# Optimization experiments

Measured on AMD Instinct MI355X. Metric: run time of the kernel, lower is better.

## Reference

```python
import jax, jax.numpy as jnp
import numpy as np

B, N, D, H = 4, 256, 256, 8
HD = D // H
DFF = 4 * D
EPS = 1e-5


def setup_inputs() -> dict:
    key = jax.random.key(0)
    ks = jax.random.split(key, 12)
    s = 0.02
    p = lambda k, shape: (jax.random.normal(k, shape, jnp.float32) * s)
    return dict(
        h=jax.random.normal(ks[0], (B, N, D), jnp.float32),
        e=jax.random.normal(ks[1], (B, N, N, D), jnp.float32),
        We=p(ks[2], (D, D)), be=jnp.zeros((D,), jnp.float32),
        Ws=p(ks[3], (D, D)), bs=jnp.zeros((D,), jnp.float32),
        Wd=p(ks[4], (D, D)), bd=jnp.zeros((D,), jnp.float32),
        Wb=p(ks[5], (D, H)), bb=jnp.zeros((H,), jnp.float32),
        ln1_g=jnp.ones((D,), jnp.float32), ln1_b=jnp.zeros((D,), jnp.float32),
        Wqkv=p(ks[6], (D, 3 * D)), bqkv=jnp.zeros((3 * D,), jnp.float32),
        Wo=p(ks[7], (D, D)), bo=jnp.zeros((D,), jnp.float32),
        ln2_g=jnp.ones((D,), jnp.float32), ln2_b=jnp.zeros((D,), jnp.float32),
        W1=p(ks[8], (D, DFF)), b1=jnp.zeros((DFF,), jnp.float32),
        W2=p(ks[9], (DFF, D)), b2=jnp.zeros((D,), jnp.float32),
    )


def _ln(x, g, b):
    m = jnp.mean(x, axis=-1, keepdims=True)
    v = jnp.mean((x - m) ** 2, axis=-1, keepdims=True)
    return (x - m) * jax.lax.rsqrt(v + EPS) * g + b


def reference(h, e, We, be, Ws, bs, Wd, bd, Wb, bb, ln1_g, ln1_b,
              Wqkv, bqkv, Wo, bo, ln2_g, ln2_b, W1, b1, W2, b2):
    # Edge update: broadcast-add of src/dst node projections + ReLU over [B,N,N,D]
    e_new = jax.nn.relu(e @ We + be
                        + (h @ Ws + bs)[:, :, None, :]   # src -> unsqueeze(2)
                        + (h @ Wd + bd)[:, None, :, :])  # dst -> unsqueeze(1)
    # Per-head additive attention bias [B,H,N,N]
    bias = jnp.einsum('bijd,dh->bhij', e_new, Wb) + bb[None, :, None, None]
    # Pre-LN self-attention with additive bias (torch MHA, eval mode)
    x = _ln(h, ln1_g, ln1_b)
    qkv = x @ Wqkv + bqkv
    q, k, v = jnp.split(qkv, 3, axis=-1)
    q = q.reshape(B, N, H, HD)
    k = k.reshape(B, N, H, HD)
    v = v.reshape(B, N, H, HD)
    scores = jnp.einsum('bihd,bjhd->bhij', q, k) / np.float32(np.sqrt(HD)) + bias
    attn = jax.nn.softmax(scores, axis=-1)
    o = jnp.einsum('bhij,bjhd->bihd', attn, v).reshape(B, N, D)
    h1 = h + (o @ Wo + bo)
    # Pre-LN FFN (exact GELU, as torch nn.GELU default)
    y = _ln(h1, ln2_g, ln2_b)
    h2 = h1 + (jax.nn.gelu(y @ W1 + b1, approximate=False) @ W2 + b2)
    return (h2, e_new)
```

## Files before the change

kernel.cpp:

```cpp
#include <hip/hip_runtime.h>
#include <math.h>

#define EPS 1e-5f

typedef __attribute__((ext_vector_type(4))) float floatx4;
typedef __attribute__((ext_vector_type(8))) short shortx8;

__device__ __forceinline__ unsigned short f2bf(float f){
  union { float f; unsigned u; } v; v.f = f;
  unsigned r = v.u + 0x7FFFu + ((v.u >> 16) & 1u);
  return (unsigned short)(r >> 16);
}
__device__ __forceinline__ float bf2f(unsigned short s){
  union { unsigned u; float f; } v; v.u = ((unsigned)s) << 16;
  return v.f;
}

__global__ __launch_bounds__(256) void k_prep(
    const float* __restrict__ We, const float* __restrict__ Ws, const float* __restrict__ Wd,
    const float* __restrict__ Wqkv, const float* __restrict__ Wo, const float* __restrict__ W1,
    const float* __restrict__ W2, const float* __restrict__ Wb,
    unsigned short* __restrict__ WeT, unsigned short* __restrict__ WsT,
    unsigned short* __restrict__ WdT, unsigned short* __restrict__ WqkvT,
    unsigned short* __restrict__ WoT, unsigned short* __restrict__ W1T,
    unsigned short* __restrict__ W2T, unsigned short* __restrict__ WbT16)
{
  const int blk = blockIdx.x, tid = threadIdx.x;
  if (blk == 240){
#pragma unroll
    for (int hh=0; hh<8; hh++) WbT16[hh*256+tid] = f2bf(Wb[tid*8+hh]);
#pragma unroll
    for (int hh=8; hh<16; hh++) WbT16[hh*256+tid] = 0;
    return;
  }
  const float* src; unsigned short* dst; int K, N, t;
  if (blk < 16)      { src=We;   dst=WeT;   K=256;  N=256;  t=blk; }
  else if (blk < 32) { src=Ws;   dst=WsT;   K=256;  N=256;  t=blk-16; }
  else if (blk < 48) { src=Wd;   dst=WdT;   K=256;  N=256;  t=blk-32; }
  else if (blk < 96) { src=Wqkv; dst=WqkvT; K=256;  N=768;  t=blk-48; }
  else if (blk < 112){ src=Wo;   dst=WoT;   K=256;  N=256;  t=blk-96; }
  else if (blk < 176){ src=W1;   dst=W1T;   K=256;  N=1024; t=blk-112; }
  else               { src=W2;   dst=W2T;   K=1024; N=256;  t=blk-176; }
  const int tpr = N >> 6;
  const int k0 = (t / tpr) << 6, n0 = (t % tpr) << 6;
  __shared__ float tile[64][65];
#pragma unroll
  for (int s=0;s<16;s++){ int f=tid+(s<<8); int r=f>>6, c=f&63;
    tile[r][c] = src[(size_t)(k0+r)*N + n0 + c]; }
  __syncthreads();
#pragma unroll
  for (int s=0;s<16;s++){ int f=tid+(s<<8); int r=f>>6, c=f&63;
    dst[(size_t)(n0+r)*K + k0 + c] = f2bf(tile[c][r]); }
}

__global__ __launch_bounds__(256) void k_front(
  const float* __restrict__ h, const float* __restrict__ g1, const float* __restrict__ b1l,
  const float* __restrict__ bs, const float* __restrict__ be, const float* __restrict__ bd,
  const float* __restrict__ bqkv,
  const unsigned short* __restrict__ WsT, const unsigned short* __restrict__ WdT,
  const unsigned short* __restrict__ WqkvT,
  float* __restrict__ S, float* __restrict__ T,
  unsigned short* __restrict__ Qb, unsigned short* __restrict__ Kb,
  unsigned short* __restrict__ VTb)
{
  __shared__ float hs[16][256];
  __shared__ __align__(16) unsigned short xa[16*264];
  __shared__ float red1[16][16], red2[16][16];
  __shared__ float rmean[16], rinv[16];
  const int tid = threadIdx.x;
  const int rb = blockIdx.x & 63;
  const int chunk = blockIdx.x >> 6;
  const int row0 = rb * 16;
  const int b = row0 >> 8;
  const int w = tid>>6, l = tid&63, lrow = l&15, quad = l>>4;

#pragma unroll
  for (int s=0;s<4;s++){
    int f = tid + s*256; int r = f>>6, c4 = f&63;
    float4 v = ((const float4*)(h + (size_t)row0*256))[f];
    *(float4*)(&hs[r][c4*4]) = v;
  }
  __syncthreads();
  {
    int row = tid>>4, l16 = tid&15;
    if (chunk >= 2){
      float sm=0.f, sq=0.f;
#pragma unroll
      for (int j=0;j<16;j++){ float v=hs[row][l16*16+j]; sm+=v; sq+=v*v; }
      red1[row][l16]=sm; red2[row][l16]=sq;
      __syncthreads();
      if (l16==0){
        float s0=0.f,q0=0.f;
#pragma unroll
        for(int k=0;k<16;k++){ s0+=red1[row][k]; q0+=red2[row][k]; }
        float m=s0*(1.f/256.f);
        rmean[row]=m; rinv[row]=rsqrtf(q0*(1.f/256.f)-m*m+EPS);
      }
      __syncthreads();
      float m=rmean[row], iv=rinv[row];
#pragma unroll
      for (int j=0;j<16;j++){ int col=l16*16+j;
        xa[row*264+col] = f2bf((hs[row][col]-m)*iv*g1[col] + b1l[col]); }
    } else {
#pragma unroll
      for (int j=0;j<16;j++){ int col=l16*16+j; xa[row*264+col] = f2bf(hs[row][col]); }
    }
  }
  __syncthreads();
  const unsigned short* Wt;
  if (chunk==0) Wt = WsT; else if (chunk==1) Wt = WdT;
  else Wt = WqkvT + (size_t)(chunk-2)*256*256;
  floatx4 a4[4];
#pragma unroll
  for (int t=0;t<4;t++) a4[t] = (floatx4){0.f,0.f,0.f,0.f};
  for (int c=0;c<8;c++){
    shortx8 af = *(const shortx8*)(xa + lrow*264 + c*32 + quad*8);
#pragma unroll
    for (int t=0;t<4;t++){
      int n = (w*4+t)*16 + lrow;
      shortx8 bf = *(const shortx8*)(Wt + (size_t)n*256 + c*32 + quad*8);
      a4[t] = __builtin_amdgcn_mfma_f32_16x16x32_bf16(af, bf, a4[t], 0, 0, 0);
    }
  }
#pragma unroll
  for (int t=0;t<4;t++){
    int ct = w*4+t;
#pragma unroll
    for (int reg=0;reg<4;reg++){
      int row = quad*4+reg, col = ct*16+lrow;
      float v = a4[t][reg];
      if (chunk==0) S[(size_t)(row0+row)*256+col] = v + bs[col] + be[col];
      else if (chunk==1) T[(size_t)(row0+row)*256+col] = v + bd[col];
      else if (chunk==2){ float q = v + bqkv[col]; int hh=col>>5, d=col&31;
        Qb[((size_t)(b*8+hh)*256 + (row0&255)+row)*32 + d] = f2bf(q); }
      else if (chunk==3){ float q = v + bqkv[256+col]; int hh=col>>5, d=col&31;
        Kb[((size_t)(b*8+hh)*256 + (row0&255)+row)*32 + d] = f2bf(q); }
      else { float q = v + bqkv[512+col]; int hh=col>>5, d=col&31;
        VTb[((size_t)(b*8+hh)*32 + d)*256 + (row0&255)+row] = f2bf(q); }
    }
  }
}

__global__ __launch_bounds__(256) void k_edge(
    const float* __restrict__ e, const unsigned short* __restrict__ WeT,
    const float* __restrict__ S, const float* __restrict__ T,
    const unsigned short* __restrict__ WbTg,
    float* __restrict__ eo, float* __restrict__ bias)
{
  __shared__ __align__(16) unsigned short smem[16896];
  __shared__ float sbuf[256];
  __shared__ __align__(16) unsigned short WbT[4096];
  unsigned short* As = smem;
  unsigned short* Bs = smem + 2560;
  unsigned short* En = smem;

  const int tid = threadIdx.x;
  const int blk = blockIdx.x;
  const int jt = blk & 3;
  const int i  = (blk >> 2) & 255;
  const int b  = blk >> 10;
  const int j0 = jt * 64;
  const int w = tid >> 6, l = tid & 63;
  const int lrow = l & 15, quad = l >> 4;

  sbuf[tid] = S[((b << 8) + i) * 256 + tid];
  ((uint4*)WbT)[tid]       = ((const uint4*)WbTg)[tid];
  ((uint4*)WbT)[tid + 256] = ((const uint4*)WbTg)[tid + 256];

  floatx4 acc[16];
#pragma unroll
  for (int t = 0; t < 16; t++) acc[t] = (floatx4){0.f,0.f,0.f,0.f};

  const float* eBase = e + ((size_t)((b*256 + i)*256 + j0)) * 256;
  const int rA = tid >> 3, qA = tid & 7;
  const int nB0 = tid >> 2, segB = tid & 2 ? 0 : 0; (void)segB;

  float4 pa0 = *(const float4*)(eBase + rA*256 + qA*4);
  float4 pa1 = *(const float4*)(eBase + (rA+32)*256 + qA*4);
  uint4 pb[4];
#pragma unroll
  for (int s=0;s<4;s++){ int f = tid + s*256; int n = f>>2, seg = f&3;
    pb[s] = *(const uint4*)(WeT + n*256 + seg*8); }
  {
    unsigned short* d0 = As + rA*40 + qA*4;
    d0[0]=f2bf(pa0.x); d0[1]=f2bf(pa0.y); d0[2]=f2bf(pa0.z); d0[3]=f2bf(pa0.w);
    unsigned short* d1 = As + (rA+32)*40 + qA*4;
    d1[0]=f2bf(pa1.x); d1[1]=f2bf(pa1.y); d1[2]=f2bf(pa1.z); d1[3]=f2bf(pa1.w);
#pragma unroll
    for (int s=0;s<4;s++){ int f = tid + s*256; int n = f>>2, seg = f&3;
      *(uint4*)(Bs + n*40 + seg*8) = pb[s]; }
  }
  __syncthreads();

  for (int c = 0; c < 8; c++){
    if (c < 7){
      const int k0n = (c+1)*32;
      pa0 = *(const float4*)(eBase + rA*256 + k0n + qA*4);
      pa1 = *(const float4*)(eBase + (rA+32)*256 + k0n + qA*4);
#pragma unroll
      for (int s=0;s<4;s++){ int f = tid + s*256; int n = f>>2, seg = f&3;
        pb[s] = *(const uint4*)(WeT + n*256 + k0n + seg*8); }
    }
    shortx8 af = *(const shortx8*)(As + (w*16 + lrow)*40 + quad*8);
#pragma unroll
    for (int t = 0; t < 16; t++){
      shortx8 bfr = *(const shortx8*)(Bs + (t*16 + lrow)*40 + quad*8);
      acc[t] = __builtin_amdgcn_mfma_f32_16x16x32_bf16(af, bfr, acc[t], 0, 0, 0);
    }
    __syncthreads();
    if (c < 7){
      unsigned short* d0 = As + rA*40 + qA*4;
      d0[0]=f2bf(pa0.x); d0[1]=f2bf(pa0.y); d0[2]=f2bf(pa0.z); d0[3]=f2bf(pa0.w);
      unsigned short* d1 = As + (rA+32)*40 + qA*4;
      d1[0]=f2bf(pa1.x); d1[1]=f2bf(pa1.y); d1[2]=f2bf(pa1.z); d1[3]=f2bf(pa1.w);
#pragma unroll
      for (int s=0;s<4;s++){ int f = tid + s*256; int n = f>>2, seg = f&3;
        *(uint4*)(Bs + n*40 + seg*8) = pb[s]; }
    }
    __syncthreads();
  }
  const float* Tb = T + (size_t)(b*256 + j0) * 256;
#pragma unroll
  for (int reg = 0; reg < 4; reg++){
    int rloc = w*16 + quad*4 + reg;
    const float* Trow = Tb + rloc*256;
#pragma unroll
    for (int t = 0; t < 16; t++){
      int col = t*16 + lrow;
      float v = acc[t][reg] + sbuf[col] + Trow[col];
      v = fmaxf(v, 0.f);
      En[rloc*264 + col] = f2bf(v);
    }
  }
  __syncthreads();
  float* eop = eo + ((size_t)((b*256 + i)*256 + j0)) * 256;
#pragma unroll
  for (int s = 0; s < 16; s++){
    int fi = tid + s*256;
    int r = fi >> 6, c4 = fi & 63;
    const unsigned short* src = En + r*264 + c4*4;
    float4 v = { bf2f(src[0]), bf2f(src[1]), bf2f(src[2]), bf2f(src[3]) };
    *(float4*)(eop + r*256 + c4*4) = v;
  }
  floatx4 accb = (floatx4){0.f,0.f,0.f,0.f};
#pragma unroll
  for (int c = 0; c < 8; c++){
    int k0 = c*32;
    shortx8 af = *(const shortx8*)(En + (w*16 + lrow)*264 + k0 + quad*8);
    shortx8 bfrag = *(const shortx8*)(WbT + lrow*256 + k0 + quad*8);
    accb = __builtin_amdgcn_mfma_f32_16x16x32_bf16(af, bfrag, accb, 0, 0, 0);
  }
  if (lrow < 8){
    float* bp = bias + ((size_t)((b*8 + lrow)*256 + i)) * 256;
    int jb = j0 + w*16 + quad*4;
#pragma unroll
    for (int r = 0; r < 4; r++) bp[jb + r] = accb[r];
  }
}


__global__ __launch_bounds__(256) void k_attn(
  const unsigned short* __restrict__ Qb, const unsigned short* __restrict__ Kb,
  const unsigned short* __restrict__ VTb, const float* __restrict__ bias,
  const float* __restrict__ bbv, unsigned short* __restrict__ Ob)
{
  __shared__ __align__(16) unsigned short Qa[32*40];
  __shared__ __align__(16) unsigned short Kl[256*40];
  __shared__ __align__(16) unsigned short Vt[32*264];
  __shared__ __align__(16) unsigned short Pl[32*264];
  __shared__ float srowm[4][16], srows[4][16], sinv[32];

  const int tid = threadIdx.x;
  const int ic = blockIdx.x & 7, bh = blockIdx.x >> 3;
  const int i0 = ic * 32;
  const int w = tid>>6, l = tid&63, lrow = l&15, quad = l>>4;

  if (tid < 128){
    int r = tid>>2, cseg = tid&3;
    *(uint4*)(Qa + r*40 + cseg*8) = ((const uint4*)(Qb + (size_t)(bh*256+i0)*32))[tid];
  }
#pragma unroll
  for (int s=0;s<4;s++){
    int f = tid + s*256; int r = f>>2, cseg = f&3;
    *(uint4*)(Kl + r*40 + cseg*8) = ((const uint4*)(Kb + (size_t)bh*8192))[f];
  }
#pragma unroll
  for (int s=0;s<4;s++){
    int f = tid + s*256; int r = f>>5, c8 = f&31;
    *(uint4*)(Vt + r*264 + c8*8) = ((const uint4*)(VTb + (size_t)bh*8192))[f];
  }
  __syncthreads();

  const int rt = w & 1, cs = (w>>1)*8;
  const float bbh = bbv[bh & 7];
  floatx4 sc[8];
  {
    shortx8 aq = *(const shortx8*)(Qa + (rt*16+lrow)*40 + quad*8);
    floatx4 z = (floatx4){0.f,0.f,0.f,0.f};
#pragma unroll
    for (int t=0;t<8;t++){
      shortx8 bk = *(const shortx8*)(Kl + ((cs+t)*16+lrow)*40 + quad*8);
      sc[t] = __builtin_amdgcn_mfma_f32_16x16x32_bf16(aq, bk, z, 0, 0, 0);
    }
  }
  const float scale = 0.17677669529663687f;
  float mx[4] = {-1e30f,-1e30f,-1e30f,-1e30f};
#pragma unroll
  for (int t=0;t<8;t++){
#pragma unroll
    for (int reg=0;reg<4;reg++){
      size_t bidx = ((size_t)(bh*256 + i0 + rt*16 + quad*4 + reg))*256 + (cs+t)*16 + lrow;
      float v = sc[t][reg]*scale + bias[bidx] + bbh;
      sc[t][reg] = v;
      mx[reg] = fmaxf(mx[reg], v);
    }
  }
#pragma unroll
  for (int m=1;m<16;m<<=1){
#pragma unroll
    for (int reg=0;reg<4;reg++) mx[reg] = fmaxf(mx[reg], __shfl_xor(mx[reg], m));
  }
  if (lrow == 0){
#pragma unroll
    for (int reg=0;reg<4;reg++) srowm[w][quad*4+reg] = mx[reg];
  }
  __syncthreads();
  float sum[4] = {0.f,0.f,0.f,0.f};
#pragma unroll
  for (int reg=0;reg<4;reg++){
    float gm = fmaxf(srowm[w][quad*4+reg], srowm[w^2][quad*4+reg]);
#pragma unroll
    for (int t=0;t<8;t++){
      float p = __expf(sc[t][reg] - gm);
      sc[t][reg] = p; sum[reg] += p;
    }
  }
#pragma unroll
  for (int m=1;m<16;m<<=1){
#pragma unroll
    for (int reg=0;reg<4;reg++) sum[reg] += __shfl_xor(sum[reg], m);
  }
  if (lrow == 0){
#pragma unroll
    for (int reg=0;reg<4;reg++) srows[w][quad*4+reg] = sum[reg];
  }
#pragma unroll
  for (int t=0;t<8;t++){
#pragma unroll
    for (int reg=0;reg<4;reg++)
      Pl[(rt*16+quad*4+reg)*264 + (cs+t)*16 + lrow] = f2bf(sc[t][reg]);
  }
  __syncthreads();
  if (lrow == 0 && w < 2){
#pragma unroll
    for (int reg=0;reg<4;reg++){
      int row = rt*16 + quad*4 + reg;
      sinv[row] = 1.f/(srows[w][quad*4+reg] + srows[w^2][quad*4+reg]);
    }
  }
  __syncthreads();
  const int rt2 = w & 1, ctd = w >> 1;
  floatx4 oc = (floatx4){0.f,0.f,0.f,0.f};
#pragma unroll
  for (int kc=0;kc<8;kc++){
    shortx8 ap = *(const shortx8*)(Pl + (rt2*16+lrow)*264 + kc*32 + quad*8);
    shortx8 bv = *(const shortx8*)(Vt + (ctd*16+lrow)*264 + kc*32 + quad*8);
    oc = __builtin_amdgcn_mfma_f32_16x16x32_bf16(ap, bv, oc, 0, 0, 0);
  }
  const int bq = bh >> 3, hh = bh & 7;
#pragma unroll
  for (int reg=0;reg<4;reg++){
    int row = rt2*16 + quad*4 + reg;
    int d = ctd*16 + lrow;
    Ob[((size_t)(bq*256 + i0 + row))*256 + hh*32 + d] = f2bf(oc[reg]*sinv[row]);
  }
}

__global__ __launch_bounds__(256) void k_back(
  const unsigned short* __restrict__ Ob, const unsigned short* __restrict__ WoT,
  const float* __restrict__ bo, const float* __restrict__ h,
  const float* __restrict__ g2, const float* __restrict__ b2l,
  const unsigned short* __restrict__ W1T, const float* __restrict__ b1f,
  const unsigned short* __restrict__ W2T, const float* __restrict__ b2f,
  float* __restrict__ out)
{
  __shared__ __align__(16) unsigned short Os[16*264];
  __shared__ float h1s[16*264];
  __shared__ __align__(16) unsigned short ys[16*264];
  __shared__ __align__(16) unsigned short Gs[16*1032];
  __shared__ float red1[16][16], red2[16][16];
  __shared__ float rmean[16], rinv[16];

  const int tid = threadIdx.x;
  const int row0 = blockIdx.x * 16;
  const int w = tid>>6, l = tid&63, lrow = l&15, quad = l>>4;

#pragma unroll
  for (int s=0;s<2;s++){
    int f = tid + s*256; int r = f>>5, c8 = f&31;
    *(uint4*)(Os + r*264 + c8*8) = ((const uint4*)(Ob + (size_t)row0*256))[f];
  }
  __syncthreads();
  {
    floatx4 a4[4];
#pragma unroll
    for (int t=0;t<4;t++) a4[t] = (floatx4){0.f,0.f,0.f,0.f};
    for (int c=0;c<8;c++){
      shortx8 af = *(const shortx8*)(Os + lrow*264 + c*32 + quad*8);
#pragma unroll
      for (int t=0;t<4;t++){
        int n = (w*4+t)*16 + lrow;
        shortx8 bf = *(const shortx8*)(WoT + (size_t)n*256 + c*32 + quad*8);
        a4[t] = __builtin_amdgcn_mfma_f32_16x16x32_bf16(af, bf, a4[t], 0, 0, 0);
      }
    }
#pragma unroll
    for (int t=0;t<4;t++){
#pragma unroll
      for (int reg=0;reg<4;reg++){
        int row = quad*4+reg, col = (w*4+t)*16+lrow;
        h1s[row*264+col] = a4[t][reg] + bo[col] + h[(size_t)(row0+row)*256 + col];
      }
    }
  }
  __syncthreads();
  {
    int row = tid>>4, l16 = tid&15;
    float sm=0.f, sq=0.f;
#pragma unroll
    for (int j=0;j<16;j++){ float v = h1s[row*264 + l16*16 + j]; sm+=v; sq+=v*v; }
    red1[row][l16]=sm; red2[row][l16]=sq;
    __syncthreads();
    if (l16==0){
      float s0=0.f,q0=0.f;
#pragma unroll
      for (int k=0;k<16;k++){ s0+=red1[row][k]; q0+=red2[row][k]; }
      float m = s0*(1.f/256.f);
      rmean[row]=m; rinv[row]=rsqrtf(q0*(1.f/256.f)-m*m+EPS);
    }
    __syncthreads();
    float m = rmean[row], iv = rinv[row];
#pragma unroll
    for (int j=0;j<16;j++){ int col = l16*16+j;
      ys[row*264+col] = f2bf((h1s[row*264+col]-m)*iv*g2[col] + b2l[col]); }
  }
  __syncthreads();
  {
    floatx4 a4[16];
#pragma unroll
    for (int t=0;t<16;t++) a4[t] = (floatx4){0.f,0.f,0.f,0.f};
    for (int c=0;c<8;c++){
      shortx8 af = *(const shortx8*)(ys + lrow*264 + c*32 + quad*8);
#pragma unroll
      for (int t=0;t<16;t++){
        int n = (w*16+t)*16 + lrow;
        shortx8 bf = *(const shortx8*)(W1T + (size_t)n*256 + c*32 + quad*8);
        a4[t] = __builtin_amdgcn_mfma_f32_16x16x32_bf16(af, bf, a4[t], 0, 0, 0);
      }
    }
#pragma unroll
    for (int t=0;t<16;t++){
#pragma unroll
      for (int reg=0;reg<4;reg++){
        int row = quad*4+reg, col = (w*16+t)*16+lrow;
        float v = a4[t][reg] + b1f[col];
        float ge = 0.5f*v*(1.f + erff(v*0.70710678118654752f));
        Gs[row*1032+col] = f2bf(ge);
      }
    }
  }
  __syncthreads();
  {
    floatx4 a4[4];
#pragma unroll
    for (int t=0;t<4;t++) a4[t] = (floatx4){0.f,0.f,0.f,0.f};
    for (int c=0;c<32;c++){
      shortx8 af = *(const shortx8*)(Gs + lrow*1032 + c*32 + quad*8);
#pragma unroll
      for (int t=0;t<4;t++){
        int n = (w*4+t)*16 + lrow;
        shortx8 bf = *(const shortx8*)(W2T + (size_t)n*1024 + c*32 + quad*8);
        a4[t] = __builtin_amdgcn_mfma_f32_16x16x32_bf16(af, bf, a4[t], 0, 0, 0);
      }
    }
#pragma unroll
    for (int t=0;t<4;t++){
#pragma unroll
      for (int reg=0;reg<4;reg++){
        int row = quad*4+reg, col = (w*4+t)*16+lrow;
        out[(size_t)(row0+row)*256+col] = h1s[row*264+col] + a4[t][reg] + b2f[col];
      }
    }
  }
}

extern "C" void kernel_launch(void* const* d_in, const int* in_sizes, int n_in,
                              void* d_out, int out_size, void* d_ws, size_t ws_size,
                              hipStream_t stream)
{
  (void)in_sizes; (void)n_in; (void)out_size; (void)ws_size;
  const float* h    = (const float*)d_in[0];
  const float* e    = (const float*)d_in[1];
  const float* We   = (const float*)d_in[2];
  const float* be   = (const float*)d_in[3];
  const float* Ws   = (const float*)d_in[4];
  const float* bs   = (const float*)d_in[5];
  const float* Wd   = (const float*)d_in[6];
  const float* bd   = (const float*)d_in[7];
  const float* Wb   = (const float*)d_in[8];
  const float* bb   = (const float*)d_in[9];
  const float* g1   = (const float*)d_in[10];
  const float* b1l  = (const float*)d_in[11];
  const float* Wqkv = (const float*)d_in[12];
  const float* bqkv = (const float*)d_in[13];
  const float* Wo   = (const float*)d_in[14];
  const float* bo   = (const float*)d_in[15];
  const float* g2   = (const float*)d_in[16];
  const float* b2l  = (const float*)d_in[17];
  const float* W1   = (const float*)d_in[18];
  const float* b1f  = (const float*)d_in[19];
  const float* W2   = (const float*)d_in[20];
  const float* b2f  = (const float*)d_in[21];

  float* out  = (float*)d_out;
  float* h2_o = out;
  float* e_o  = out + 262144;

  float* wsf = (float*)d_ws;
  unsigned short* ush = (unsigned short*)d_ws;
  unsigned short* WeT   = ush;
  unsigned short* WsT   = ush + 65536;
  unsigned short* WdT   = ush + 131072;
  unsigned short* WqkvT = ush + 196608;
  unsigned short* WoT   = ush + 393216;
  unsigned short* W1T   = ush + 458752;
  unsigned short* W2T   = ush + 720896;
  unsigned short* WbT16 = ush + 983040;
  float* S_   = wsf + 493568;
  float* T_   = wsf + 755712;
  float* bias = wsf + 1017856;
  unsigned short* Qb  = (unsigned short*)(wsf + 3115008);
  unsigned short* Kb  = (unsigned short*)(wsf + 3246080);
  unsigned short* VTb = (unsigned short*)(wsf + 3377152);
  unsigned short* Ob  = (unsigned short*)(wsf + 3508224);

  k_prep <<<dim3(241),  dim3(256), 0, stream>>>(We,Ws,Wd,Wqkv,Wo,W1,W2,Wb,
                                                WeT,WsT,WdT,WqkvT,WoT,W1T,W2T,WbT16);
  k_front<<<dim3(320),  dim3(256), 0, stream>>>(h, g1,b1l, bs,be,bd, bqkv,
                                                WsT,WdT,WqkvT, S_,T_, Qb,Kb,VTb);
  k_edge <<<dim3(4096), dim3(256), 0, stream>>>(e, WeT, S_, T_, WbT16, e_o, bias);
  k_attn <<<dim3(256),  dim3(256), 0, stream>>>(Qb, Kb, VTb, bias, bb, Ob);
  k_back <<<dim3(64),   dim3(256), 0, stream>>>(Ob, WoT, bo, h, g2,b2l,
                                                W1T,b1f, W2T,b2f, h2_o);
}
```

Before: 668.6 us.

## Stream edge tiles straight into MFMA registers without LDS staging in k_edge

Rewrites the edge GEMM so each lane loads its own fp32 slice of e, converts it to bf16 in registers and uses it directly as the MFMA operand. The bf16 weight fragments are read straight from global memory instead of being staged in shared memory. With the operand roles swapped, each lane owns contiguous output columns, so the ReLU'd edge output is written as fp32 float4 with no bf16 round-trip through LDS, and the block-wide barriers disappear. LDS shrinks to the per-wave bias tile and launch bounds request 3 blocks per CU; the cost is strided per-lane global loads and repeated weight reads that rely on cache hits.

```diff
diff --git a/kernel.cpp b/kernel.cpp
--- a/kernel.cpp
+++ b/kernel.cpp
@@ -141,18 +141,13 @@
   }
 }
 
-__global__ __launch_bounds__(256) void k_edge(
+__global__ __launch_bounds__(256, 3) void k_edge(
     const float* __restrict__ e, const unsigned short* __restrict__ WeT,
     const float* __restrict__ S, const float* __restrict__ T,
     const unsigned short* __restrict__ WbTg,
     float* __restrict__ eo, float* __restrict__ bias)
 {
-  __shared__ __align__(16) unsigned short smem[16896];
-  __shared__ float sbuf[256];
-  __shared__ __align__(16) unsigned short WbT[4096];
-  unsigned short* As = smem;
-  unsigned short* Bs = smem + 2560;
-  unsigned short* En = smem;
+  __shared__ __align__(16) unsigned short En[64*264];
 
   const int tid = threadIdx.x;
   const int blk = blockIdx.x;
@@ -162,92 +157,60 @@
   const int j0 = jt * 64;
   const int w = tid >> 6, l = tid & 63;
   const int lrow = l & 15, quad = l >> 4;
-
-  sbuf[tid] = S[((b << 8) + i) * 256 + tid];
-  ((uint4*)WbT)[tid]       = ((const uint4*)WbTg)[tid];
-  ((uint4*)WbT)[tid + 256] = ((const uint4*)WbTg)[tid + 256];
+  const int jloc = w*16 + lrow;
+
+  const float* eRow = e + ((size_t)((b*256 + i)*256 + j0 + jloc)) * 256 + quad*8;
+  const float* Trow = T + ((size_t)(b*256 + j0 + jloc)) * 256;
+  const float* Srow = S + ((size_t)(b*256 + i)) * 256;
+  const unsigned short* wBase = WeT + lrow*256 + quad*8;
 
   floatx4 acc[16];
 #pragma unroll
   for (int t = 0; t < 16; t++) acc[t] = (floatx4){0.f,0.f,0.f,0.f};
 
-  const float* eBase = e + ((size_t)((b*256 + i)*256 + j0)) * 256;
-  const int rA = tid >> 3, qA = tid & 7;
-  const int nB0 = tid >> 2, segB = tid & 2 ? 0 : 0; (void)segB;
-
-  float4 pa0 = *(const float4*)(eBase + rA*256 + qA*4);
-  float4 pa1 = *(const float4*)(eBase + (rA+32)*256 + qA*4);
-  uint4 pb[4];
-#pragma unroll
-  for (int s=0;s<4;s++){ int f = tid + s*256; int n = f>>2, seg = f&3;
-    pb[s] = *(const uint4*)(WeT + n*256 + seg*8); }
-  {
-    unsigned short* d0 = As + rA*40 + qA*4;
-    d0[0]=f2bf(pa0.x); d0[1]=f2bf(pa0.y); d0[2]=f2bf(pa0.z); d0[3]=f2bf(pa0.w);
-    unsigned short* d1 = As + (rA+32)*40 + qA*4;
-    d1[0]=f2bf(pa1.x); d1[1]=f2bf(pa1.y); d1[2]=f2bf(pa1.z); d1[3]=f2bf(pa1.w);
-#pragma unroll
-    for (int s=0;s<4;s++){ int f = tid + s*256; int n = f>>2, seg = f&3;
-      *(uint4*)(Bs + n*40 + seg*8) = pb[s]; }
-  }
-  __syncthreads();
-
-  for (int c = 0; c < 8; c++){
+  float4 e0 = *(const float4*)(eRow);
+  float4 e1 = *(const float4*)(eRow + 4);
+
+  for (int c = 0; c < 8; ++c){
+    shortx8 ef;
+    ef[0]=f2bf(e0.x); ef[1]=f2bf(e0.y); ef[2]=f2bf(e0.z); ef[3]=f2bf(e0.w);
+    ef[4]=f2bf(e1.x); ef[5]=f2bf(e1.y); ef[6]=f2bf(e1.z); ef[7]=f2bf(e1.w);
     if (c < 7){
-      const int k0n = (c+1)*32;
-      pa0 = *(const float4*)(eBase + rA*256 + k0n + qA*4);
-      pa1 = *(const float4*)(eBase + (rA+32)*256 + k0n + qA*4);
-#pragma unroll
-      for (int s=0;s<4;s++){ int f = tid + s*256; int n = f>>2, seg = f&3;
-        pb[s] = *(const uint4*)(WeT + n*256 + k0n + seg*8); }
-    }
-    shortx8 af = *(const shortx8*)(As + (w*16 + lrow)*40 + quad*8);
-#pragma unroll
-    for (int t = 0; t < 16; t++){
-      shortx8 bfr = *(const shortx8*)(Bs + (t*16 + lrow)*40 + quad*8);
-      acc[t] = __builtin_amdgcn_mfma_f32_16x16x32_bf16(af, bfr, acc[t], 0, 0, 0);
-    }
-    __syncthreads();
-    if (c < 7){
-      unsigned short* d0 = As + rA*40 + qA*4;
-      d0[0]=f2bf(pa0.x); d0[1]=f2bf(pa0.y); d0[2]=f2bf(pa0.z); d0[3]=f2bf(pa0.w);
-      unsigned short* d1 = As + (rA+32)*40 + qA*4;
-      d1[0]=f2bf(pa1.x); d1[1]=f2bf(pa1.y); d1[2]=f2bf(pa1.z); d1[3]=f2bf(pa1.w);
-#pragma unroll
-      for (int s=0;s<4;s++){ int f = tid + s*256; int n = f>>2, seg = f&3;
-        *(uint4*)(Bs + n*40 + seg*8) = pb[s]; }
-    }
-    __syncthreads();
-  }
-  const float* Tb = T + (size_t)(b*256 + j0) * 256;
-#pragma unroll
-  for (int reg = 0; reg < 4; reg++){
-    int rloc = w*16 + quad*4 + reg;
-    const float* Trow = Tb + rloc*256;
-#pragma unroll
-    for (int t = 0; t < 16; t++){
-      int col = t*16 + lrow;
-      float v = acc[t][reg] + sbuf[col] + Trow[col];
-      v = fmaxf(v, 0.f);
-      En[rloc*264 + col] = f2bf(v);
-    }
-  }
-  __syncthreads();
-  float* eop = eo + ((size_t)((b*256 + i)*256 + j0)) * 256;
-#pragma unroll
-  for (int s = 0; s < 16; s++){
-    int fi = tid + s*256;
-    int r = fi >> 6, c4 = fi & 63;
-    const unsigned short* src = En + r*264 + c4*4;
-    float4 v = { bf2f(src[0]), bf2f(src[1]), bf2f(src[2]), bf2f(src[3]) };
-    *(float4*)(eop + r*256 + c4*4) = v;
-  }
+      e0 = *(const float4*)(eRow + (c+1)*32);
+      e1 = *(const float4*)(eRow + (c+1)*32 + 4);
+    }
+    const unsigned short* wp = wBase + c*32;
+#pragma unroll
+    for (int t = 0; t < 16; ++t){
+      shortx8 wf = *(const shortx8*)(wp + t*4096);
+      acc[t] = __builtin_amdgcn_mfma_f32_16x16x32_bf16(wf, ef, acc[t], 0, 0, 0);
+    }
+  }
+
+  float* eop = eo + ((size_t)((b*256 + i)*256 + j0 + jloc)) * 256;
+#pragma unroll
+  for (int t = 0; t < 16; ++t){
+    const int d0 = t*16 + quad*4;
+    float4 sv = *(const float4*)(Srow + d0);
+    float4 tv = *(const float4*)(Trow + d0);
+    float v0 = fmaxf(acc[t][0] + sv.x + tv.x, 0.f);
+    float v1 = fmaxf(acc[t][1] + sv.y + tv.y, 0.f);
+    float v2 = fmaxf(acc[t][2] + sv.z + tv.z, 0.f);
+    float v3 = fmaxf(acc[t][3] + sv.w + tv.w, 0.f);
+    float4 ov; ov.x = v0; ov.y = v1; ov.z = v2; ov.w = v3;
+    *(float4*)(eop + d0) = ov;
+    uint2 pk;
+    pk.x = (unsigned int)f2bf(v0) | ((unsigned int)f2bf(v1) << 16);
+    pk.y = (unsigned int)f2bf(v2) | ((unsigned int)f2bf(v3) << 16);
+    *(uint2*)(En + jloc*264 + d0) = pk;
+  }
+
   floatx4 accb = (floatx4){0.f,0.f,0.f,0.f};
 #pragma unroll
   for (int c = 0; c < 8; c++){
     int k0 = c*32;
-    shortx8 af = *(const shortx8*)(En + (w*16 + lrow)*264 + k0 + quad*8);
-    shortx8 bfrag = *(const shortx8*)(WbT + lrow*256 + k0 + quad*8);
+    shortx8 af = *(const shortx8*)(En + jloc*264 + k0 + quad*8);
+    shortx8 bfrag = *(const shortx8*)(WbTg + lrow*256 + k0 + quad*8);
     accb = __builtin_amdgcn_mfma_f32_16x16x32_bf16(af, bfrag, accb, 0, 0, 0);
   }
   if (lrow < 8){
@@ -257,7 +220,6 @@
     for (int r = 0; r < 4; r++) bp[jb + r] = accb[r];
   }
 }
-
 
 __global__ __launch_bounds__(256) void k_attn(
   const unsigned short* __restrict__ Qb, const unsigned short* __restrict__ Kb,
```

New measurement: 783.4 us. 17.2% more time.
